# Kernel optimization log

Measured on AMD Instinct MI355X. Metric: run time of the kernel, lower is better.

Reference implementation:

```python
import jax, jax.numpy as jnp
import numpy as np
from jax import lax

EPS = 1e-06
K = 7  # kernel_size
C1 = 0.01 ** 2
C2 = 0.03 ** 2

_SOBEL_X = jnp.array([[-1.0, 0.0, 1.0], [-2.0, 0.0, 2.0], [-1.0, 0.0, 1.0]], dtype=jnp.float32).reshape(1, 1, 3, 3)
_SOBEL_Y = jnp.array([[-1.0, -2.0, -1.0], [0.0, 0.0, 0.0], [1.0, 2.0, 1.0]], dtype=jnp.float32).reshape(1, 1, 3, 3)


def _conv3x3(x, w):
    # NCHW cross-correlation with zero padding=1 (matches F.conv2d)
    return lax.conv_general_dilated(
        x, w, window_strides=(1, 1), padding=[(1, 1), (1, 1)],
        dimension_numbers=('NCHW', 'OIHW', 'NCHW'))


def _box(x):
    # avg_pool2d(k, stride=1, pad=k//2, count_include_pad=True):
    # sum over zero-padded window, divide by k*k everywhere.
    p = K // 2
    s = lax.reduce_window(x, jnp.float32(0.0), lax.add,
                          window_dimensions=(1, 1, K, K),
                          window_strides=(1, 1, 1, 1),
                          padding=[(0, 0), (0, 0), (p, p), (p, p)])
    return s / jnp.float32(K * K)


def _grad_mag(x):
    gx = _conv3x3(x, _SOBEL_X)
    gy = _conv3x3(x, _SOBEL_Y)
    return jnp.sqrt(gx * gx + gy * gy + EPS)


def setup_inputs() -> dict:
    key = jax.random.key(0)
    k1, k2 = jax.random.split(key)
    B, H, W = 64, 512, 512
    pred = jax.random.normal(k1, (B, 1, H, W), dtype=jnp.float32)
    target = jax.random.normal(k2, (B, 1, H, W), dtype=jnp.float32)
    min_target = jnp.zeros((B,), dtype=jnp.float32)
    max_target = jnp.ones((B,), dtype=jnp.float32)
    return {"pred": pred, "target": target, "min_target": min_target, "max_target": max_target}


def reference(pred, target, min_target, max_target):
    B = pred.shape[0]
    mn = min_target.reshape(B, 1, 1, 1)
    mx = max_target.reshape(B, 1, 1, 1)
    dr = jnp.maximum(mx - mn, EPS)
    p = (pred - mn) / dr
    t = (target - mn) / dr

    gp = _grad_mag(p)
    gt = _grad_mag(t)

    mu_p = _box(p)
    mu_t = _box(t)
    luminance = (2.0 * mu_p * mu_t + C1) / (mu_p * mu_p + mu_t * mu_t + C1)

    mu_gp = _box(gp)
    mu_gt = _box(gt)
    sig_p = _box(gp * gp) - mu_gp * mu_gp
    sig_t = _box(gt * gt) - mu_gt * mu_gt
    sig_x = _box(gp * gt) - mu_gp * mu_gt
    cs = (2.0 * sig_x + C2) / (sig_p + sig_t + C2)

    return 1.0 - jnp.mean(luminance * cs)
```

## Files before the change

### kernel.cpp

```cpp
#include <hip/hip_runtime.h>
#include <hip/hip_fp16.h>
#include <math.h>


constexpr int NT = 256;
constexpr float EPS_F = 1e-6f;
constexpr float C1S = 2401.0f * 0.0001f;
constexpr float C2S = 2401.0f * 0.0009f;

union U4 { uint4 u; __half2 h[4]; };
union F4U { float4 v; float a[4]; };

__device__ __forceinline__ __half2 h2swap(__half2 x) {
    unsigned u = __builtin_bit_cast(unsigned, x);
    u = (u >> 16) | (u << 16);
    return __builtin_bit_cast(__half2, u);
}

__device__ __forceinline__ float ssim_px(__half2 apt, __half2 ag, __half2 agg, __half2 agx) {
    float2 vpt = __half22float2(apt);
    float2 vg  = __half22float2(ag);
    float2 vgg = __half22float2(agg);
    float  vgx = __low2float(agx);
    float lum_n = 2.0f * vpt.x * vpt.y + C1S;
    float lum_d = vpt.x * vpt.x + vpt.y * vpt.y + C1S;
    float cs_n  = 2.0f * (49.0f * vgx - vg.x * vg.y) + C2S;
    float cs_d  = 49.0f * (vgg.x + vgg.y) - vg.x * vg.x - vg.y * vg.y + C2S;
    return lum_n * cs_n * __builtin_amdgcn_rcpf(lum_d) * __builtin_amdgcn_rcpf(cs_d);
}

__global__ __launch_bounds__(NT, 4)
void gssim_strip(const float* __restrict__ pred, const float* __restrict__ target,
                 const float* __restrict__ mn_arr, const float* __restrict__ mx_arr,
                 float* __restrict__ partial) {
    constexpr int H = 512, W = 512;
    __shared__ alignas(16) __half2 spt[40][44];
    __shared__ alignas(16) __half2 sg[38][44];
    __shared__ alignas(16) __half2 hsAll[32][41][4];
    __shared__ float red[4];

    const int blk = blockIdx.x;
    const int b   = blk >> 4;
    const int gy0 = (blk & 15) * 32;
    const int tid = threadIdx.x;

    const float mn     = mn_arr[b];
    const float inv_dr = 1.0f / fmaxf(mx_arr[b] - mn, EPS_F);
    const float* pimg = pred   + (size_t)b * H * W;
    const float* timg = target + (size_t)b * H * W;

    const int y0 = tid / 10, g0 = tid - y0 * 10;
    const int i1 = tid + 256;
    const int y1 = i1 / 10,  g1 = i1 - y1 * 10;
    const bool has2 = (tid < 144);
    const int gyA = gy0 - 4 + y0;
    const int gyB = gy0 - 4 + y1;
    const bool rowAok = (gyA >= 0 && gyA < H);
    const bool rowBok = (gyB >= 0 && gyB < H);

    F4U P0, T0, P1, T1;

    auto stage1 = [&](int gx0n, int g, bool rowok, int gyI, F4U& P, F4U& T) {
        int gx = gx0n - 4 + 4 * g;
        P.v = make_float4(0.f, 0.f, 0.f, 0.f);
        T.v = make_float4(0.f, 0.f, 0.f, 0.f);
        if (rowok) {
            if (gx >= 0 && gx + 4 <= W) {
                P.v = *reinterpret_cast<const float4*>(pimg + (size_t)gyI * W + gx);
                T.v = *reinterpret_cast<const float4*>(timg + (size_t)gyI * W + gx);
            } else {
#pragma unroll
                for (int c = 0; c < 4; ++c) {
                    int x = gx + c;
                    if (x >= 0 && x < W) {
                        P.a[c] = pimg[(size_t)gyI * W + x];
                        T.a[c] = timg[(size_t)gyI * W + x];
                    }
                }
            }
        }
    };

    auto writeA = [&](F4U& P, F4U& T, int y, int g, bool rowok, int gx0n) {
        int gx = gx0n - 4 + 4 * g;
        U4 w;
#pragma unroll
        for (int c = 0; c < 4; ++c) {
            int x = gx + c;
            bool ok = rowok && (x >= 0) && (x < W);
            float pv = ok ? (P.a[c] - mn) * inv_dr : 0.f;
            float tv = ok ? (T.a[c] - mn) * inv_dr : 0.f;
            w.h[c] = __floats2half2_rn(pv, tv);
        }
        *reinterpret_cast<uint4*>(&spt[y][4 * g]) = w.u;
    };

    stage1(0, g0, rowAok, gyA, P0, T0);
    if (has2) stage1(0, g1, rowBok, gyB, P1, T1);

    const __half2 two2  = __float2half2_rn(2.0f);
    const __half2 eps2  = __float2half2_rn(1e-6f);
    const __half2 zero2 = __float2half2_rn(0.0f);

    float accl = 0.0f;

    for (int tx = 0; tx < 16; ++tx) {
        const int gx0 = tx * 32;

        writeA(P0, T0, y0, g0, rowAok, gx0);
        if (has2) writeA(P1, T1, y1, g1, rowBok, gx0);
        __syncthreads();

        if (tx < 15) {
            stage1(gx0 + 32, g0, rowAok, gyA, P0, T0);
            if (has2) stage1(gx0 + 32, g1, rowBok, gyB, P1, T1);
        }

        for (int i = tid; i < 380; i += NT) {
            int k = i / 10, g = i - k * 10;
            int j0 = 4 * g;
            U4 w; w.h[0] = zero2; w.h[1] = zero2; w.h[2] = zero2; w.h[3] = zero2;
            int gr = gy0 + k - 3;
            if (gr >= 0 && gr < H) {
                __half2 a[3][6];
#pragma unroll
                for (int r = 0; r < 3; ++r) {
                    U4 v; v.u = *reinterpret_cast<const uint4*>(&spt[k + r][j0]);
                    a[r][0] = v.h[0]; a[r][1] = v.h[1]; a[r][2] = v.h[2]; a[r][3] = v.h[3];
                    uint2 v2 = *reinterpret_cast<const uint2*>(&spt[k + r][j0 + 4]);
                    a[r][4] = __builtin_bit_cast(__half2, v2.x);
                    a[r][5] = __builtin_bit_cast(__half2, v2.y);
                }
#pragma unroll
                for (int c = 0; c < 4; ++c) {
                    __half2 gxh = __hsub2(a[0][c + 2], a[0][c]);
                    gxh = __hfma2(two2, __hsub2(a[1][c + 2], a[1][c]), gxh);
                    gxh = __hadd2(gxh, __hsub2(a[2][c + 2], a[2][c]));
                    __half2 gyh = __hsub2(a[2][c], a[0][c]);
                    gyh = __hfma2(two2, __hsub2(a[2][c + 1], a[0][c + 1]), gyh);
                    gyh = __hadd2(gyh, __hsub2(a[2][c + 2], a[0][c + 2]));
                    __half2 m2 = __hfma2(gxh, gxh, __hfma2(gyh, gyh, eps2));
                    __half2 mag = h2sqrt(m2);
                    int gc = gx0 + j0 + c - 3;
                    w.h[c] = (gc >= 0 && gc < W) ? mag : zero2;
                }
            }
            *reinterpret_cast<uint4*>(&sg[k][j0]) = w.u;
        }
        __syncthreads();

        for (int i = tid; i < 304; i += NT) {
            int cg = i / 38;
            int k  = i - cg * 38;
            int c0 = 4 * cg;
            __half2 ptv[12], sgv[12];
#pragma unroll
            for (int q = 0; q < 3; ++q) {
                U4 v; v.u = *reinterpret_cast<const uint4*>(&spt[k + 1][c0 + 4 * q]);
                ptv[4 * q] = v.h[0]; ptv[4 * q + 1] = v.h[1]; ptv[4 * q + 2] = v.h[2]; ptv[4 * q + 3] = v.h[3];
                U4 u; u.u = *reinterpret_cast<const uint4*>(&sg[k][c0 + 4 * q]);
                sgv[4 * q] = u.h[0]; sgv[4 * q + 1] = u.h[1]; sgv[4 * q + 2] = u.h[2]; sgv[4 * q + 3] = u.h[3];
            }
            __half2 gg[10], gx2[10];
#pragma unroll
            for (int q = 0; q < 10; ++q) {
                gg[q]  = __hmul2(sgv[q], sgv[q]);
                gx2[q] = __hmul2(sgv[q], h2swap(sgv[q]));
            }
            __half2 Hpt = ptv[1], Hg = sgv[0], Hgg = gg[0], Hgx = gx2[0];
#pragma unroll
            for (int q = 1; q < 7; ++q) {
                Hpt = __hadd2(Hpt, ptv[q + 1]);
                Hg  = __hadd2(Hg,  sgv[q]);
                Hgg = __hadd2(Hgg, gg[q]);
                Hgx = __hadd2(Hgx, gx2[q]);
            }
            U4 w0;
            w0.h[0] = Hpt; w0.h[1] = Hg; w0.h[2] = Hgg; w0.h[3] = Hgx;
            *reinterpret_cast<uint4*>(&hsAll[c0][k][0]) = w0.u;
#pragma unroll
            for (int m = 1; m < 4; ++m) {
                Hpt = __hadd2(__hsub2(Hpt, ptv[m]),      ptv[m + 7]);
                Hg  = __hadd2(__hsub2(Hg,  sgv[m - 1]),  sgv[m + 6]);
                Hgg = __hadd2(__hsub2(Hgg, gg[m - 1]),   gg[m + 6]);
                Hgx = __hadd2(__hsub2(Hgx, gx2[m - 1]),  gx2[m + 6]);
                U4 w;
                w.h[0] = Hpt; w.h[1] = Hg; w.h[2] = Hgg; w.h[3] = Hgx;
                *reinterpret_cast<uint4*>(&hsAll[c0 + m][k][0]) = w.u;
            }
        }
        __syncthreads();

        {
            const int ox = tid & 31;
            const int q  = tid >> 5;
            const int r0 = 4 * q;
            U4 win[10];
#pragma unroll
            for (int j = 0; j < 7; ++j)
                win[j].u = *reinterpret_cast<const uint4*>(&hsAll[ox][r0 + j][0]);
            __half2 Spt = win[0].h[0], Sg = win[0].h[1], Sgg = win[0].h[2], Sgx = win[0].h[3];
#pragma unroll
            for (int j = 1; j < 7; ++j) {
                Spt = __hadd2(Spt, win[j].h[0]);
                Sg  = __hadd2(Sg,  win[j].h[1]);
                Sgg = __hadd2(Sgg, win[j].h[2]);
                Sgx = __hadd2(Sgx, win[j].h[3]);
            }
            accl += ssim_px(Spt, Sg, Sgg, Sgx);
#pragma unroll
            for (int s = 1; s < 4; ++s) {
                win[6 + s].u = *reinterpret_cast<const uint4*>(&hsAll[ox][r0 + 6 + s][0]);
                Spt = __hadd2(__hsub2(Spt, win[s - 1].h[0]), win[6 + s].h[0]);
                Sg  = __hadd2(__hsub2(Sg,  win[s - 1].h[1]), win[6 + s].h[1]);
                Sgg = __hadd2(__hsub2(Sgg, win[s - 1].h[2]), win[6 + s].h[2]);
                Sgx = __hadd2(__hsub2(Sgx, win[s - 1].h[3]), win[6 + s].h[3]);
                accl += ssim_px(Spt, Sg, Sgg, Sgx);
            }
        }
        __syncthreads();
    }

#pragma unroll
    for (int off = 32; off > 0; off >>= 1) accl += __shfl_down(accl, off, 64);
    if ((tid & 63) == 0) red[tid >> 6] = accl;
    __syncthreads();
    if (tid == 0) partial[blk] = red[0] + red[1] + red[2] + red[3];
}

__global__ __launch_bounds__(256)
void gssim_final(const float* __restrict__ partial, int n,
                 float* __restrict__ out, double inv_count) {
    __shared__ double sred[256];
    double acc = 0.0;
    for (int i = threadIdx.x; i < n; i += 256) acc += (double)partial[i];
    sred[threadIdx.x] = acc;
    __syncthreads();
    for (int s = 128; s > 0; s >>= 1) {
        if ((int)threadIdx.x < s) sred[threadIdx.x] += sred[threadIdx.x + s];
        __syncthreads();
    }
    if (threadIdx.x == 0) out[0] = (float)(1.0 - sred[0] * inv_count);
}

extern "C" void kernel_launch(void* const* d_in, const int* in_sizes, int n_in,
                              void* d_out, int out_size, void* d_ws, size_t ws_size,
                              hipStream_t stream) {
    const float* pred   = (const float*)d_in[0];
    const float* target = (const float*)d_in[1];
    const float* mn     = (const float*)d_in[2];
    const float* mx     = (const float*)d_in[3];
    float* out = (float*)d_out;

    const int B = in_sizes[2];
    const int H = 512, W = 512;

    float* partial = (float*)d_ws;

    const int nblocks = B * (H / 32);
    gssim_strip<<<nblocks, NT, 0, stream>>>(pred, target, mn, mx, partial);

    const double inv_count = 1.0 / ((double)B * (double)H * (double)W);
    gssim_final<<<1, 256, 0, stream>>>(partial, nblocks, out, inv_count);
}
```

Measured before the change: 81.73 us.

## Give each thread two rows per stage and move next tile's shared write earlier

```diff
diff --git a/kernel.cpp b/kernel.cpp
--- a/kernel.cpp
+++ b/kernel.cpp
@@ -49,19 +49,19 @@
     const float* pimg = pred   + (size_t)b * H * W;
     const float* timg = target + (size_t)b * H * W;
 
-    const int y0 = tid / 10, g0 = tid - y0 * 10;
-    const int i1 = tid + 256;
-    const int y1 = i1 / 10,  g1 = i1 - y1 * 10;
-    const bool has2 = (tid < 144);
-    const int gyA = gy0 - 4 + y0;
-    const int gyB = gy0 - 4 + y1;
-    const bool rowAok = (gyA >= 0 && gyA < H);
-    const bool rowBok = (gyB >= 0 && gyB < H);
-
-    F4U P0, T0, P1, T1;
-
-    auto stage1 = [&](int gx0n, int g, bool rowok, int gyI, F4U& P, F4U& T) {
-        int gx = gx0n - 4 + 4 * g;
+    const int gS  = tid % 10;
+    const int yr  = tid / 10;
+    const int yS0 = 2 * yr, yS1 = yS0 + 1;
+    const int gyS0 = gy0 - 4 + yS0;
+    const int gyS1 = gyS0 + 1;
+    const bool rok0 = (gyS0 >= 0 && gyS0 < H);
+    const bool rok1 = (gyS1 >= 0 && gyS1 < H);
+    const bool hasS = (tid < 200);
+
+    F4U Pa0, Ta0, Pa1, Ta1;
+
+    auto stage1 = [&](int gx0n, bool rowok, int gyI, F4U& P, F4U& T) {
+        int gx = gx0n - 4 + 4 * gS;
         P.v = make_float4(0.f, 0.f, 0.f, 0.f);
         T.v = make_float4(0.f, 0.f, 0.f, 0.f);
         if (rowok) {
@@ -80,9 +80,13 @@
             }
         }
     };
-
-    auto writeA = [&](F4U& P, F4U& T, int y, int g, bool rowok, int gx0n) {
-        int gx = gx0n - 4 + 4 * g;
+    auto stagePair = [&](int gx0n) {
+        stage1(gx0n, rok0, gyS0, Pa0, Ta0);
+        stage1(gx0n, rok1, gyS1, Pa1, Ta1);
+    };
+
+    auto writeOne = [&](F4U& P, F4U& T, int y, bool rowok, int gx0n) {
+        int gx = gx0n - 4 + 4 * gS;
         U4 w;
 #pragma unroll
         for (int c = 0; c < 4; ++c) {
@@ -92,101 +96,110 @@
             float tv = ok ? (T.a[c] - mn) * inv_dr : 0.f;
             w.h[c] = __floats2half2_rn(pv, tv);
         }
-        *reinterpret_cast<uint4*>(&spt[y][4 * g]) = w.u;
-    };
-
-    stage1(0, g0, rowAok, gyA, P0, T0);
-    if (has2) stage1(0, g1, rowBok, gyB, P1, T1);
+        *reinterpret_cast<uint4*>(&spt[y][4 * gS]) = w.u;
+    };
+    auto writePair = [&](int gx0n) {
+        writeOne(Pa0, Ta0, yS0, rok0, gx0n);
+        writeOne(Pa1, Ta1, yS1, rok1, gx0n);
+    };
 
     const __half2 two2  = __float2half2_rn(2.0f);
     const __half2 eps2  = __float2half2_rn(1e-6f);
     const __half2 zero2 = __float2half2_rn(0.0f);
 
+    if (hasS) { stagePair(0); writePair(0); }
+    __syncthreads();
+
     float accl = 0.0f;
 
     for (int tx = 0; tx < 16; ++tx) {
         const int gx0 = tx * 32;
 
-        writeA(P0, T0, y0, g0, rowAok, gx0);
-        if (has2) writeA(P1, T1, y1, g1, rowBok, gx0);
-        __syncthreads();
-
-        if (tx < 15) {
-            stage1(gx0 + 32, g0, rowAok, gyA, P0, T0);
-            if (has2) stage1(gx0 + 32, g1, rowBok, gyB, P1, T1);
-        }
-
-        for (int i = tid; i < 380; i += NT) {
-            int k = i / 10, g = i - k * 10;
-            int j0 = 4 * g;
-            U4 w; w.h[0] = zero2; w.h[1] = zero2; w.h[2] = zero2; w.h[3] = zero2;
-            int gr = gy0 + k - 3;
-            if (gr >= 0 && gr < H) {
-                __half2 a[3][6];
-#pragma unroll
-                for (int r = 0; r < 3; ++r) {
-                    U4 v; v.u = *reinterpret_cast<const uint4*>(&spt[k + r][j0]);
-                    a[r][0] = v.h[0]; a[r][1] = v.h[1]; a[r][2] = v.h[2]; a[r][3] = v.h[3];
-                    uint2 v2 = *reinterpret_cast<const uint2*>(&spt[k + r][j0 + 4]);
-                    a[r][4] = __builtin_bit_cast(__half2, v2.x);
-                    a[r][5] = __builtin_bit_cast(__half2, v2.y);
-                }
-#pragma unroll
-                for (int c = 0; c < 4; ++c) {
-                    __half2 gxh = __hsub2(a[0][c + 2], a[0][c]);
-                    gxh = __hfma2(two2, __hsub2(a[1][c + 2], a[1][c]), gxh);
-                    gxh = __hadd2(gxh, __hsub2(a[2][c + 2], a[2][c]));
-                    __half2 gyh = __hsub2(a[2][c], a[0][c]);
-                    gyh = __hfma2(two2, __hsub2(a[2][c + 1], a[0][c + 1]), gyh);
-                    gyh = __hadd2(gyh, __hsub2(a[2][c + 2], a[0][c + 2]));
-                    __half2 m2 = __hfma2(gxh, gxh, __hfma2(gyh, gyh, eps2));
-                    __half2 mag = h2sqrt(m2);
-                    int gc = gx0 + j0 + c - 3;
-                    w.h[c] = (gc >= 0 && gc < W) ? mag : zero2;
-                }
-            }
-            *reinterpret_cast<uint4*>(&sg[k][j0]) = w.u;
-        }
-        __syncthreads();
-
-        for (int i = tid; i < 304; i += NT) {
-            int cg = i / 38;
-            int k  = i - cg * 38;
-            int c0 = 4 * cg;
-            __half2 ptv[12], sgv[12];
-#pragma unroll
-            for (int q = 0; q < 3; ++q) {
-                U4 v; v.u = *reinterpret_cast<const uint4*>(&spt[k + 1][c0 + 4 * q]);
-                ptv[4 * q] = v.h[0]; ptv[4 * q + 1] = v.h[1]; ptv[4 * q + 2] = v.h[2]; ptv[4 * q + 3] = v.h[3];
-                U4 u; u.u = *reinterpret_cast<const uint4*>(&sg[k][c0 + 4 * q]);
-                sgv[4 * q] = u.h[0]; sgv[4 * q + 1] = u.h[1]; sgv[4 * q + 2] = u.h[2]; sgv[4 * q + 3] = u.h[3];
-            }
-            __half2 gg[10], gx2[10];
-#pragma unroll
-            for (int q = 0; q < 10; ++q) {
-                gg[q]  = __hmul2(sgv[q], sgv[q]);
-                gx2[q] = __hmul2(sgv[q], h2swap(sgv[q]));
-            }
-            __half2 Hpt = ptv[1], Hg = sgv[0], Hgg = gg[0], Hgx = gx2[0];
-#pragma unroll
-            for (int q = 1; q < 7; ++q) {
-                Hpt = __hadd2(Hpt, ptv[q + 1]);
-                Hg  = __hadd2(Hg,  sgv[q]);
-                Hgg = __hadd2(Hgg, gg[q]);
-                Hgx = __hadd2(Hgx, gx2[q]);
-            }
-            U4 w0;
-            w0.h[0] = Hpt; w0.h[1] = Hg; w0.h[2] = Hgg; w0.h[3] = Hgx;
-            *reinterpret_cast<uint4*>(&hsAll[c0][k][0]) = w0.u;
-#pragma unroll
-            for (int m = 1; m < 4; ++m) {
-                Hpt = __hadd2(__hsub2(Hpt, ptv[m]),      ptv[m + 7]);
-                Hg  = __hadd2(__hsub2(Hg,  sgv[m - 1]),  sgv[m + 6]);
-                Hgg = __hadd2(__hsub2(Hgg, gg[m - 1]),   gg[m + 6]);
-                Hgx = __hadd2(__hsub2(Hgx, gx2[m - 1]),  gx2[m + 6]);
-                U4 w;
-                w.h[0] = Hpt; w.h[1] = Hg; w.h[2] = Hgg; w.h[3] = Hgx;
-                *reinterpret_cast<uint4*>(&hsAll[c0 + m][k][0]) = w.u;
+        if (tx < 15 && hasS) stagePair(gx0 + 32);
+
+        if (tid < 190) {
+            const int g  = tid % 10, kr = tid / 10;
+            const int j0 = 4 * g, k0 = 2 * kr;
+            __half2 a[4][6];
+#pragma unroll
+            for (int r = 0; r < 4; ++r) {
+                U4 v; v.u = *reinterpret_cast<const uint4*>(&spt[k0 + r][j0]);
+                a[r][0] = v.h[0]; a[r][1] = v.h[1]; a[r][2] = v.h[2]; a[r][3] = v.h[3];
+                uint2 v2 = *reinterpret_cast<const uint2*>(&spt[k0 + r][j0 + 4]);
+                a[r][4] = __builtin_bit_cast(__half2, v2.x);
+                a[r][5] = __builtin_bit_cast(__half2, v2.y);
+            }
+            bool cm[4];
+#pragma unroll
+            for (int c = 0; c < 4; ++c) {
+                int gc = gx0 + j0 + c - 3;
+                cm[c] = (gc >= 0 && gc < W);
+            }
+#pragma unroll
+            for (int rr = 0; rr < 2; ++rr) {
+                const int k = k0 + rr;
+                const int gr = gy0 + k - 3;
+                U4 w; w.h[0] = zero2; w.h[1] = zero2; w.h[2] = zero2; w.h[3] = zero2;
+                if (gr >= 0 && gr < H) {
+#pragma unroll
+                    for (int c = 0; c < 4; ++c) {
+                        __half2 gxh = __hsub2(a[rr][c + 2], a[rr][c]);
+                        gxh = __hfma2(two2, __hsub2(a[rr + 1][c + 2], a[rr + 1][c]), gxh);
+                        gxh = __hadd2(gxh, __hsub2(a[rr + 2][c + 2], a[rr + 2][c]));
+                        __half2 gyh = __hsub2(a[rr + 2][c], a[rr][c]);
+                        gyh = __hfma2(two2, __hsub2(a[rr + 2][c + 1], a[rr][c + 1]), gyh);
+                        gyh = __hadd2(gyh, __hsub2(a[rr + 2][c + 2], a[rr][c + 2]));
+                        __half2 m2 = __hfma2(gxh, gxh, __hfma2(gyh, gyh, eps2));
+                        __half2 mag = h2sqrt(m2);
+                        w.h[c] = cm[c] ? mag : zero2;
+                    }
+                }
+                *reinterpret_cast<uint4*>(&sg[k][j0]) = w.u;
+            }
+        }
+        __syncthreads();
+
+        if (tid < 152) {
+            const int kr = tid % 19, cg = tid / 19;
+            const int c0 = 4 * cg;
+#pragma unroll
+            for (int rr = 0; rr < 2; ++rr) {
+                const int k = 2 * kr + rr;
+                __half2 ptv[12], sgv[12];
+#pragma unroll
+                for (int q = 0; q < 3; ++q) {
+                    U4 v; v.u = *reinterpret_cast<const uint4*>(&spt[k + 1][c0 + 4 * q]);
+                    ptv[4 * q] = v.h[0]; ptv[4 * q + 1] = v.h[1]; ptv[4 * q + 2] = v.h[2]; ptv[4 * q + 3] = v.h[3];
+                    U4 u; u.u = *reinterpret_cast<const uint4*>(&sg[k][c0 + 4 * q]);
+                    sgv[4 * q] = u.h[0]; sgv[4 * q + 1] = u.h[1]; sgv[4 * q + 2] = u.h[2]; sgv[4 * q + 3] = u.h[3];
+                }
+                __half2 gg[10], gx2[10];
+#pragma unroll
+                for (int q = 0; q < 10; ++q) {
+                    gg[q]  = __hmul2(sgv[q], sgv[q]);
+                    gx2[q] = __hmul2(sgv[q], h2swap(sgv[q]));
+                }
+                __half2 Hpt = ptv[1], Hg = sgv[0], Hgg = gg[0], Hgx = gx2[0];
+#pragma unroll
+                for (int q = 1; q < 7; ++q) {
+                    Hpt = __hadd2(Hpt, ptv[q + 1]);
+                    Hg  = __hadd2(Hg,  sgv[q]);
+                    Hgg = __hadd2(Hgg, gg[q]);
+                    Hgx = __hadd2(Hgx, gx2[q]);
+                }
+                U4 w0;
+                w0.h[0] = Hpt; w0.h[1] = Hg; w0.h[2] = Hgg; w0.h[3] = Hgx;
+                *reinterpret_cast<uint4*>(&hsAll[c0][k][0]) = w0.u;
+#pragma unroll
+                for (int m = 1; m < 4; ++m) {
+                    Hpt = __hadd2(__hsub2(Hpt, ptv[m]),      ptv[m + 7]);
+                    Hg  = __hadd2(__hsub2(Hg,  sgv[m - 1]),  sgv[m + 6]);
+                    Hgg = __hadd2(__hsub2(Hgg, gg[m - 1]),   gg[m + 6]);
+                    Hgx = __hadd2(__hsub2(Hgx, gx2[m - 1]),  gx2[m + 6]);
+                    U4 w;
+                    w.h[0] = Hpt; w.h[1] = Hg; w.h[2] = Hgg; w.h[3] = Hgx;
+                    *reinterpret_cast<uint4*>(&hsAll[c0 + m][k][0]) = w.u;
+                }
             }
         }
         __syncthreads();
@@ -218,6 +231,8 @@
                 accl += ssim_px(Spt, Sg, Sgg, Sgx);
             }
         }
+
+        if (tx < 15 && hasS) writePair(gx0 + 32);
         __syncthreads();
     }
 
```

Result: faster. 79.81 us (-2.3%).
